# Performance work log

Hardware: AMD Instinct MI355X
Metric: run time of the kernel (lower is better)

The kernel has to match this reference:

```python
import jax, jax.numpy as jnp
import numpy as np

E_NUM, R_NUM, D, B = 100000, 200, 128, 4096


def setup_inputs() -> dict:
    key = jax.random.key(0)
    k = jax.random.split(key, 7)
    return {
        "h": jax.random.randint(k[0], (B,), 0, E_NUM),
        "r": jax.random.randint(k[1], (B,), 0, R_NUM),
        "pos_t": jax.random.randint(k[2], (B,), 0, E_NUM),
        "neg_t": jax.random.randint(k[3], (B,), 0, E_NUM),
        # xavier-normal-ish init scales
        "entity_embed": jax.random.normal(k[4], (E_NUM, D), jnp.float32) * 0.12,
        "relation_embed": jax.random.normal(k[5], (R_NUM, D), jnp.float32) * 0.12,
        "trans_M": jax.random.normal(k[6], (R_NUM, D * D), jnp.float32) * 0.011,
    }


def reference(h, r, pos_t, neg_t, entity_embed, relation_embed, trans_M):
    h_e = entity_embed[h]            # [B, D]
    pos_e = entity_embed[pos_t]      # [B, D]
    neg_e = entity_embed[neg_t]      # [B, D]
    r_e = relation_embed[r]          # [B, D]
    W_r = trans_M[r].reshape(-1, D, D)  # [B, D, D]
    # row-vector @ matrix per sample: (1xD) @ (DxD) -> D
    trans_h = jnp.einsum("bd,bde->be", h_e, W_r)
    trans_pos = jnp.einsum("bd,bde->be", pos_e, W_r)
    trans_neg = jnp.einsum("bd,bde->be", neg_e, W_r)
    return (trans_h, r_e, trans_pos, trans_neg)
```

## Files before the change

### kernel.cpp

```cpp
#include <hip/hip_runtime.h>

#define DDIM    128
#define NS      4
#define SCOL    32
#define SCH     21
#define MROWS   64
#define XSTRIDE 136
#define WSTRIDE 136
#define SEGCAP  96

typedef __attribute__((ext_vector_type(8))) short bf16x8;
typedef __attribute__((ext_vector_type(4))) float f32x4;

static __device__ inline unsigned short f2b(float f) {
    unsigned u = __float_as_uint(f);
    u += 0x7fff + ((u >> 16) & 1);
    return (unsigned short)(u >> 16);
}

__global__ __launch_bounds__(256) void transr_mfma(
    const int* __restrict__ h, const int* __restrict__ r,
    const int* __restrict__ pos_t, const int* __restrict__ neg_t,
    const float* __restrict__ ent, const float* __restrict__ rel,
    const float* __restrict__ M, float* __restrict__ out,
    int B, int R)
{
    const int bid  = blockIdx.x;
    const int rb   = bid % R;
    const int qc   = bid / R;
    const int t    = threadIdx.x;
    const int wvid = t >> 6;
    const int ln   = t & 63;

    __shared__ __align__(16) unsigned short Xl[MROWS * XSTRIDE];
    __shared__ __align__(16) unsigned short Wt[SCOL  * WSTRIDE];
    __shared__ int seg[4][SEGCAP];
    __shared__ int wcnt[4];
    __shared__ int list_s[4 * SEGCAP];

    const int g  = t >> 4;
    const int nl = t & 15;
    const float* __restrict__ Wg = M + (size_t)rb * DDIM * DDIM + qc * SCOL;
    float wreg0[8], wreg1[8];
    #pragma unroll
    for (int j = 0; j < 8; ++j) wreg0[j] = Wg[(size_t)(g * 8 + j) * DDIM + nl];
    #pragma unroll
    for (int j = 0; j < 8; ++j) wreg1[j] = Wg[(size_t)(g * 8 + j) * DDIM + nl + 16];

    int segn = 0;
    const int qlen4  = B >> 4;
    const int qbase4 = wvid * qlen4;
    const int4* __restrict__ r4 = (const int4*)r;
    for (int i0 = 0; i0 < qlen4; i0 += 64) {
        const int  e4 = qbase4 + i0 + ln;
        const int4 rv = r4[e4];
        const int  ib = e4 << 2;
        #pragma unroll
        for (int j = 0; j < 4; ++j) {
            const int  rj = (j == 0) ? rv.x : (j == 1) ? rv.y : (j == 2) ? rv.z : rv.w;
            const bool f  = (rj == rb);
            const unsigned long long m = __ballot(f);
            if (f) {
                const int p = segn + __popcll(m & ((1ull << ln) - 1ull));
                if (p < SEGCAP) seg[wvid][p] = ib + j;
            }
            segn += __popcll(m);
        }
    }
    if (ln == 0) wcnt[wvid] = min(segn, SEGCAP);

    {
        bf16x8 w0, w1;
        #pragma unroll
        for (int j = 0; j < 8; ++j) { w0[j] = (short)f2b(wreg0[j]); w1[j] = (short)f2b(wreg1[j]); }
        *(bf16x8*)(&Wt[nl * WSTRIDE + g * 8])        = w0;
        *(bf16x8*)(&Wt[(nl + 16) * WSTRIDE + g * 8]) = w1;
    }
    __syncthreads();

    const int c0 = wcnt[0], c1 = wcnt[1], c2 = wcnt[2], c3 = wcnt[3];
    const int cum1 = c0, cum2 = c0 + c1, cum3 = c0 + c1 + c2;
    const int cnt  = cum3 + c3;
    if (cnt == 0) return;

    for (int lin = t; lin < cnt; lin += 256) {
        int w, k;
        if      (lin < cum1) { w = 0; k = lin;        }
        else if (lin < cum2) { w = 1; k = lin - cum1; }
        else if (lin < cum3) { w = 2; k = lin - cum2; }
        else                 { w = 3; k = lin - cum3; }
        list_s[lin] = seg[w][k];
    }
    __syncthreads();

    const int lr = ln & 15;
    const int lg = ln >> 4;
    bf16x8 bfr0[4], bfr1[4];
    #pragma unroll
    for (int ks = 0; ks < 4; ++ks) {
        const int kg = ks * 4 + lg;
        bfr0[ks] = *(const bf16x8*)(&Wt[(0 * 16 + lr) * WSTRIDE + kg * 8]);
        bfr1[ks] = *(const bf16x8*)(&Wt[(1 * 16 + lr) * WSTRIDE + kg * 8]);
    }

    const size_t BD = (size_t)B * DDIM;
    for (int ch = 0; ch < cnt; ch += SCH) {
        const int rows_valid = 3 * min(SCH, cnt - ch);

        for (int lin = t; lin < MROWS * 16; lin += 256) {
            const int row  = lin >> 4;
            const int kg   = lin & 15;
            const int rowg = min(3 * ch + row, 3 * cnt - 1);
            const int jj   = rowg / 3;
            const int v    = rowg - 3 * jj;
            const int sidx = list_s[jj];
            const int eid  = (v == 0) ? h[sidx] : (v == 1) ? pos_t[sidx] : neg_t[sidx];
            const float4 a = *(const float4*)(ent + (size_t)eid * DDIM + kg * 8);
            const float4 b = *(const float4*)(ent + (size_t)eid * DDIM + kg * 8 + 4);
            bf16x8 x;
            x[0] = (short)f2b(a.x); x[1] = (short)f2b(a.y);
            x[2] = (short)f2b(a.z); x[3] = (short)f2b(a.w);
            x[4] = (short)f2b(b.x); x[5] = (short)f2b(b.y);
            x[6] = (short)f2b(b.z); x[7] = (short)f2b(b.w);
            *(bf16x8*)(&Xl[row * XSTRIDE + kg * 8]) = x;
        }
        __syncthreads();

        f32x4 acc0 = {0.f, 0.f, 0.f, 0.f};
        f32x4 acc1 = {0.f, 0.f, 0.f, 0.f};
        #pragma unroll
        for (int ks = 0; ks < 4; ++ks) {
            const int kg = ks * 4 + lg;
            const bf16x8 a = *(const bf16x8*)(&Xl[(wvid * 16 + lr) * XSTRIDE + kg * 8]);
            acc0 = __builtin_amdgcn_mfma_f32_16x16x32_bf16(a, bfr0[ks], acc0, 0, 0, 0);
            acc1 = __builtin_amdgcn_mfma_f32_16x16x32_bf16(a, bfr1[ks], acc1, 0, 0, 0);
        }

        #pragma unroll
        for (int q = 0; q < 4; ++q) {
            const int rowe = wvid * 16 + lg * 4 + q;
            if (rowe < rows_valid) {
                const int rg = 3 * ch + rowe;
                const int j2 = rg / 3;
                const int v2 = rg - 3 * j2;
                const size_t s = (size_t)list_s[j2];
                float* bp = (v2 == 0) ? out : (v2 == 1) ? (out + 2 * BD) : (out + 3 * BD);
                bp[s * DDIM + qc * SCOL + lr]      = acc0[q];
                bp[s * DDIM + qc * SCOL + lr + 16] = acc1[q];
            }
        }
        __syncthreads();
    }

    for (int lin = t; lin < cnt * (SCOL / 4); lin += 256) {
        const int j  = lin >> 3;
        const int c4 = lin & 7;
        const float4 v = *(const float4*)(rel + (size_t)rb * DDIM + qc * SCOL + c4 * 4);
        *(float4*)(out + (size_t)B * DDIM + (size_t)list_s[j] * DDIM + qc * SCOL + c4 * 4) = v;
    }
}

extern "C" void kernel_launch(void* const* d_in, const int* in_sizes, int n_in,
                              void* d_out, int out_size, void* d_ws, size_t ws_size,
                              hipStream_t stream) {
    const int*   h     = (const int*)d_in[0];
    const int*   r     = (const int*)d_in[1];
    const int*   pos_t = (const int*)d_in[2];
    const int*   neg_t = (const int*)d_in[3];
    const float* ent   = (const float*)d_in[4];
    const float* rel   = (const float*)d_in[5];
    const float* M     = (const float*)d_in[6];
    float*       out   = (float*)d_out;

    const int B = in_sizes[0];
    const int R = in_sizes[5] / DDIM;

    transr_mfma<<<dim3(R * NS), dim3(256), 0, stream>>>(
        h, r, pos_t, neg_t, ent, rel, M, out, B, R);
}
```

Baseline: 16.79 us.

## Split each relation's sample list across two blocks and retile waves over M/N

Doubles the grid by splitting each relation's matching samples into two halves handled by separate blocks, so more blocks run concurrently on the GPU. Each block now works on chunks of 10 samples (30 rows) instead of 21, and the four waves are retiled as 2 M-tiles by 2 N-tiles, each with one accumulator. Gather loads only touch valid rows. The cost is that every block still scans the full r array and loads its W slice, so that fixed per-block overhead is duplicated.

```diff
diff --git a/kernel.cpp b/kernel.cpp
--- a/kernel.cpp
+++ b/kernel.cpp
@@ -2,9 +2,10 @@
 
 #define DDIM    128
 #define NS      4
+#define SG      2
 #define SCOL    32
-#define SCH     21
-#define MROWS   64
+#define SCH     10
+#define MROWS   32
 #define XSTRIDE 136
 #define WSTRIDE 136
 #define SEGCAP  96
@@ -27,7 +28,9 @@
 {
     const int bid  = blockIdx.x;
     const int rb   = bid % R;
-    const int qc   = bid / R;
+    const int rest = bid / R;
+    const int qc   = rest & (NS - 1);
+    const int sg   = rest >> 2;
     const int t    = threadIdx.x;
     const int wvid = t >> 6;
     const int ln   = t & 63;
@@ -93,27 +96,42 @@
     }
     __syncthreads();
 
+    const int halfc  = (cnt + 1) >> 1;
+    const int gstart = sg * halfc;
+    const int gcnt   = max(0, min(cnt - gstart, halfc));
+
+    if (sg == 0) {
+        for (int lin = t; lin < cnt * (SCOL / 4); lin += 256) {
+            const int j  = lin >> 3;
+            const int c4 = lin & 7;
+            const float4 v = *(const float4*)(rel + (size_t)rb * DDIM + qc * SCOL + c4 * 4);
+            *(float4*)(out + (size_t)B * DDIM + (size_t)list_s[j] * DDIM + qc * SCOL + c4 * 4) = v;
+        }
+    }
+    if (gcnt == 0) return;
+
     const int lr = ln & 15;
     const int lg = ln >> 4;
-    bf16x8 bfr0[4], bfr1[4];
+    const int mt = wvid & 1;
+    const int nt = wvid >> 1;
+    bf16x8 bfr[4];
     #pragma unroll
     for (int ks = 0; ks < 4; ++ks) {
         const int kg = ks * 4 + lg;
-        bfr0[ks] = *(const bf16x8*)(&Wt[(0 * 16 + lr) * WSTRIDE + kg * 8]);
-        bfr1[ks] = *(const bf16x8*)(&Wt[(1 * 16 + lr) * WSTRIDE + kg * 8]);
+        bfr[ks] = *(const bf16x8*)(&Wt[(nt * 16 + lr) * WSTRIDE + kg * 8]);
     }
 
     const size_t BD = (size_t)B * DDIM;
-    for (int ch = 0; ch < cnt; ch += SCH) {
-        const int rows_valid = 3 * min(SCH, cnt - ch);
+    for (int ch = 0; ch < gcnt; ch += SCH) {
+        const int ccnt = min(SCH, gcnt - ch);
+        const int rows_valid = 3 * ccnt;
 
-        for (int lin = t; lin < MROWS * 16; lin += 256) {
+        for (int lin = t; lin < rows_valid * 16; lin += 256) {
             const int row  = lin >> 4;
             const int kg   = lin & 15;
-            const int rowg = min(3 * ch + row, 3 * cnt - 1);
-            const int jj   = rowg / 3;
-            const int v    = rowg - 3 * jj;
-            const int sidx = list_s[jj];
+            const int jj   = row / 3;
+            const int v    = row - 3 * jj;
+            const int sidx = list_s[gstart + ch + jj];
             const int eid  = (v == 0) ? h[sidx] : (v == 1) ? pos_t[sidx] : neg_t[sidx];
             const float4 a = *(const float4*)(ent + (size_t)eid * DDIM + kg * 8);
             const float4 b = *(const float4*)(ent + (size_t)eid * DDIM + kg * 8 + 4);
@@ -126,37 +144,26 @@
         }
         __syncthreads();
 
-        f32x4 acc0 = {0.f, 0.f, 0.f, 0.f};
-        f32x4 acc1 = {0.f, 0.f, 0.f, 0.f};
+        f32x4 acc = {0.f, 0.f, 0.f, 0.f};
         #pragma unroll
         for (int ks = 0; ks < 4; ++ks) {
             const int kg = ks * 4 + lg;
-            const bf16x8 a = *(const bf16x8*)(&Xl[(wvid * 16 + lr) * XSTRIDE + kg * 8]);
-            acc0 = __builtin_amdgcn_mfma_f32_16x16x32_bf16(a, bfr0[ks], acc0, 0, 0, 0);
-            acc1 = __builtin_amdgcn_mfma_f32_16x16x32_bf16(a, bfr1[ks], acc1, 0, 0, 0);
+            const bf16x8 a = *(const bf16x8*)(&Xl[(mt * 16 + lr) * XSTRIDE + kg * 8]);
+            acc = __builtin_amdgcn_mfma_f32_16x16x32_bf16(a, bfr[ks], acc, 0, 0, 0);
         }
 
         #pragma unroll
         for (int q = 0; q < 4; ++q) {
-            const int rowe = wvid * 16 + lg * 4 + q;
+            const int rowe = mt * 16 + lg * 4 + q;
             if (rowe < rows_valid) {
-                const int rg = 3 * ch + rowe;
-                const int j2 = rg / 3;
-                const int v2 = rg - 3 * j2;
-                const size_t s = (size_t)list_s[j2];
+                const int jj = rowe / 3;
+                const int v2 = rowe - 3 * jj;
+                const size_t s = (size_t)list_s[gstart + ch + jj];
                 float* bp = (v2 == 0) ? out : (v2 == 1) ? (out + 2 * BD) : (out + 3 * BD);
-                bp[s * DDIM + qc * SCOL + lr]      = acc0[q];
-                bp[s * DDIM + qc * SCOL + lr + 16] = acc1[q];
+                bp[s * DDIM + qc * SCOL + nt * 16 + lr] = acc[q];
             }
         }
         __syncthreads();
-    }
-
-    for (int lin = t; lin < cnt * (SCOL / 4); lin += 256) {
-        const int j  = lin >> 3;
-        const int c4 = lin & 7;
-        const float4 v = *(const float4*)(rel + (size_t)rb * DDIM + qc * SCOL + c4 * 4);
-        *(float4*)(out + (size_t)B * DDIM + (size_t)list_s[j] * DDIM + qc * SCOL + c4 * 4) = v;
     }
 }
 
@@ -175,6 +182,6 @@
     const int B = in_sizes[0];
     const int R = in_sizes[5] / DDIM;
 
-    transr_mfma<<<dim3(R * NS), dim3(256), 0, stream>>>(
+    transr_mfma<<<dim3(R * NS * SG), dim3(256), 0, stream>>>(
         h, r, pos_t, neg_t, ent, rel, M, out, B, R);
 }
```

Result: faster. 15.48 us (-7.8%).
